# Kernel optimization log

Measured on AMD Instinct MI355X. Metric: run time of the kernel, lower is better.

Reference implementation:

```python
import jax, jax.numpy as jnp
import numpy as np

N_LEVELS = 20
F = 2                      # n_features_per_level
LOG2T = 19
T = 1 << LOG2T             # hashmap size per level
BASE_RES = 16
PER_LEVEL_SCALE = 1.39
N_POINTS = 1_000_000

# 8 corner offsets of a voxel, (8, 3)
OFFSETS = np.array([[i, j, k] for i in (0, 1) for j in (0, 1) for k in (0, 1)], dtype=np.int32)
# spatial hash primes (only 3 needed for 3D input); uint32 multiply wraps like torch int32 bits
PRIME_Y = np.uint32(2654435761)
PRIME_Z = np.uint32(805459861)


def setup_inputs() -> dict:
    key = jax.random.key(0)
    k1, k2 = jax.random.split(key)
    x = jax.random.uniform(k1, (N_POINTS, 3), dtype=jnp.float32)  # points in [0,1)^3
    # nn.init.uniform_(weight, a=-1e-4, b=1e-4), one table per level, stacked
    tables = jax.random.uniform(k2, (N_LEVELS, T, F), minval=-1e-4, maxval=1e-4, dtype=jnp.float32)
    return {"x": x, "tables": tables}


def _hash(coords):
    # coords: (..., 3) int32 voxel corner indices -> (...,) int32 in [0, T)
    c = coords.astype(jnp.uint32)
    h = c[..., 0] ^ (c[..., 1] * PRIME_Y) ^ (c[..., 2] * PRIME_Z)
    return (h & jnp.uint32(T - 1)).astype(jnp.int32)


def _encode_level(x, table, resolution):
    xs = x * resolution                      # (B, 3)
    vmin = jnp.floor(xs).astype(jnp.int32)   # (B, 3)
    corners = vmin[:, None, :] + OFFSETS[None, :, :]   # (B, 8, 3)
    idx = _hash(corners)                     # (B, 8)
    e = table[idx]                           # (B, 8, F) gather
    w = xs - vmin                            # fractional position, (B, 3)
    wx, wy, wz = w[:, 0:1], w[:, 1:2], w[:, 2:3]
    # trilinear interpolation, exact lerp chain from the torch module
    c00 = e[:, 0] * (1 - wx) + e[:, 4] * wx
    c01 = e[:, 1] * (1 - wx) + e[:, 5] * wx
    c10 = e[:, 2] * (1 - wx) + e[:, 6] * wx
    c11 = e[:, 3] * (1 - wx) + e[:, 7] * wx
    c0 = c00 * (1 - wy) + c10 * wy
    c1 = c01 * (1 - wy) + c11 * wy
    return c0 * (1 - wz) + c1 * wz           # (B, F)


def reference(x, tables):
    outs = [_encode_level(x, tables[i], int(BASE_RES * PER_LEVEL_SCALE ** i))
            for i in range(N_LEVELS)]
    return jnp.concatenate(outs, axis=-1)    # (B, N_LEVELS * F) = (B, 40)
```

## Files before the change

### kernel.cpp

```cpp
#include <hip/hip_runtime.h>

#define NLEV 20
#define TSIZE (1u << 19)
#define TMASK (TSIZE - 1u)
#define PRIME_Y 2654435761u
#define PRIME_Z 805459861u

typedef float f32x2 __attribute__((ext_vector_type(2)));
typedef float f32x4 __attribute__((ext_vector_type(4)));

__device__ __constant__ int kRes[NLEV] = {
    16, 22, 30, 42, 59, 83, 115, 160, 222, 309,
    430, 598, 832, 1156, 1608, 2235, 3107, 4318, 6003, 8344};

__device__ __forceinline__ float2 encode_one(const float2* __restrict__ tbl,
                                             float r, float px, float py,
                                             float pz) {
  const float xs0 = px * r, xs1 = py * r, xs2 = pz * r;
  const float f0 = floorf(xs0), f1 = floorf(xs1), f2 = floorf(xs2);
  const float wx = xs0 - f0, wy = xs1 - f1, wz = xs2 - f2;
  const unsigned v0 = (unsigned)(int)f0;
  const unsigned v1 = (unsigned)(int)f1;
  const unsigned v2 = (unsigned)(int)f2;

  const unsigned hy0 = v1 * PRIME_Y, hy1 = (v1 + 1u) * PRIME_Y;
  const unsigned hz0 = v2 * PRIME_Z, hz1 = (v2 + 1u) * PRIME_Z;
  unsigned H[4];
  H[0] = hy0 ^ hz0;
  H[1] = hy0 ^ hz1;
  H[2] = hy1 ^ hz0;
  H[3] = hy1 ^ hz1;

  float2 e0[4], e1[4];

  if ((v0 & 1u) == 0u) {
#pragma unroll
    for (int j = 0; j < 4; ++j) {
      const unsigned i0 = (v0 ^ H[j]) & TMASK;
      const f32x4 q = *(const f32x4*)((const float*)tbl + 2u * (i0 & ~1u));
      const bool lo = (i0 & 1u) == 0u;
      e0[j] = lo ? make_float2(q.x, q.y) : make_float2(q.z, q.w);
      e1[j] = lo ? make_float2(q.z, q.w) : make_float2(q.x, q.y);
    }
  } else {
#pragma unroll
    for (int j = 0; j < 4; ++j) {
      e0[j] = tbl[(v0 ^ H[j]) & TMASK];
      e1[j] = tbl[((v0 + 1u) ^ H[j]) & TMASK];
    }
  }

  const float owx = 1.0f - wx, owy = 1.0f - wy, owz = 1.0f - wz;

  const float c00a = e0[0].x * owx + e1[0].x * wx;
  const float c01a = e0[1].x * owx + e1[1].x * wx;
  const float c10a = e0[2].x * owx + e1[2].x * wx;
  const float c11a = e0[3].x * owx + e1[3].x * wx;
  const float c0a = c00a * owy + c10a * wy;
  const float c1a = c01a * owy + c11a * wy;

  const float c00b = e0[0].y * owx + e1[0].y * wx;
  const float c01b = e0[1].y * owx + e1[1].y * wx;
  const float c10b = e0[2].y * owx + e1[2].y * wx;
  const float c11b = e0[3].y * owx + e1[3].y * wx;
  const float c0b = c00b * owy + c10b * wy;
  const float c1b = c01b * owy + c11b * wy;

  return make_float2(c0a * owz + c1a * wz, c0b * owz + c1b * wz);
}

__global__ __launch_bounds__(256) void enc_level_kernel(
    const float* __restrict__ x, const float* __restrict__ tables,
    float2* __restrict__ ws, int n) {
  const int l = blockIdx.y;
  const int p = blockIdx.x * 256 + threadIdx.x;
  if (p >= n) return;
  const float px = __builtin_nontemporal_load(x + 3 * p + 0);
  const float py = __builtin_nontemporal_load(x + 3 * p + 1);
  const float pz = __builtin_nontemporal_load(x + 3 * p + 2);
  const float2* __restrict__ tbl = (const float2*)tables + (size_t)l * TSIZE;
  const float2 v = encode_one(tbl, (float)kRes[l], px, py, pz);
  f32x2 vv;
  vv.x = v.x;
  vv.y = v.y;
  __builtin_nontemporal_store(vv, (f32x2*)(ws + (size_t)l * n + p));
}

__global__ __launch_bounds__(256) void transpose_kernel(
    const float2* __restrict__ ws, float* __restrict__ out, int n) {
  __shared__ float lds[256 * 41];
  const int p0 = blockIdx.x * 256;
  const int t = threadIdx.x;
  const int npts = min(256, n - p0);

#pragma unroll
  for (int l = 0; l < NLEV; ++l) {
    if (t < npts) {
      const f32x2 v =
          __builtin_nontemporal_load((const f32x2*)(ws + (size_t)l * n + p0 + t));
      lds[t * 41 + 2 * l + 0] = v.x;
      lds[t * 41 + 2 * l + 1] = v.y;
    }
  }
  __syncthreads();

  const int total4 = npts * 10;
  f32x4* __restrict__ dst = (f32x4*)(out + (size_t)p0 * (NLEV * 2));
#pragma unroll
  for (int k = 0; k < 10; ++k) {
    const int g = t + k * 256;
    if (g < total4) {
      const int pl = g / 10;
      const int comp = g - pl * 10;
      const float* s = &lds[pl * 41 + comp * 4];
      f32x4 v;
      v.x = s[0];
      v.y = s[1];
      v.z = s[2];
      v.w = s[3];
      dst[g] = v;
    }
  }
}

__global__ __launch_bounds__(256) void hash_enc_kernel(
    const float* __restrict__ x, const float* __restrict__ tables,
    float* __restrict__ out, int n) {
  int p = blockIdx.x * 256 + threadIdx.x;
  if (p >= n) return;
  const float px = x[3 * p + 0];
  const float py = x[3 * p + 1];
  const float pz = x[3 * p + 2];
  float o[NLEV * 2];
#pragma unroll
  for (int l = 0; l < NLEV; ++l) {
    const float2* tbl = (const float2*)tables + (size_t)l * TSIZE;
    const float2 v = encode_one(tbl, (float)kRes[l], px, py, pz);
    o[2 * l + 0] = v.x;
    o[2 * l + 1] = v.y;
  }
  float4* __restrict__ dst = (float4*)(out + (size_t)p * (NLEV * 2));
#pragma unroll
  for (int k = 0; k < 10; ++k) {
    dst[k] = make_float4(o[4 * k + 0], o[4 * k + 1], o[4 * k + 2], o[4 * k + 3]);
  }
}

extern "C" void kernel_launch(void* const* d_in, const int* in_sizes, int n_in,
                              void* d_out, int out_size, void* d_ws, size_t ws_size,
                              hipStream_t stream) {
  const float* x = (const float*)d_in[0];
  const float* tables = (const float*)d_in[1];
  float* out = (float*)d_out;
  const int n = in_sizes[0] / 3;
  const size_t ws_needed = (size_t)NLEV * n * 2 * sizeof(float);

  if (ws_size >= ws_needed) {
    const int pblocks = (n + 255) / 256;
    dim3 grid1(pblocks, NLEV);
    enc_level_kernel<<<grid1, 256, 0, stream>>>(x, tables, (float2*)d_ws, n);
    transpose_kernel<<<pblocks, 256, 0, stream>>>((const float2*)d_ws, out, n);
  } else {
    const int grid = (n + 255) / 256;
    hash_enc_kernel<<<grid, 256, 0, stream>>>(x, tables, out, n);
  }
}
```

Measured before the change: 685.7 us.

## Unify paired-corner gather path and retile transpose to 128 points per block

```diff
diff --git a/kernel.cpp b/kernel.cpp
--- a/kernel.cpp
+++ b/kernel.cpp
@@ -31,24 +31,26 @@
   H[2] = hy1 ^ hz0;
   H[3] = hy1 ^ hz1;
 
-  float2 e0[4], e1[4];
+  float2 e0[4], epair[4], e1o[4];
 
-  if ((v0 & 1u) == 0u) {
 #pragma unroll
-    for (int j = 0; j < 4; ++j) {
-      const unsigned i0 = (v0 ^ H[j]) & TMASK;
-      const f32x4 q = *(const f32x4*)((const float*)tbl + 2u * (i0 & ~1u));
-      const bool lo = (i0 & 1u) == 0u;
-      e0[j] = lo ? make_float2(q.x, q.y) : make_float2(q.z, q.w);
-      e1[j] = lo ? make_float2(q.z, q.w) : make_float2(q.x, q.y);
-    }
-  } else {
+  for (int j = 0; j < 4; ++j) {
+    const unsigned i0 = (v0 ^ H[j]) & TMASK;
+    const f32x4 q = *(const f32x4*)((const float*)tbl + 2u * (i0 & ~1u));
+    const bool lo = (i0 & 1u) == 0u;
+    e0[j] = lo ? make_float2(q.x, q.y) : make_float2(q.z, q.w);
+    epair[j] = lo ? make_float2(q.z, q.w) : make_float2(q.x, q.y);
+  }
+
+  const bool odd = (v0 & 1u) != 0u;
+  if (odd) {
 #pragma unroll
-    for (int j = 0; j < 4; ++j) {
-      e0[j] = tbl[(v0 ^ H[j]) & TMASK];
-      e1[j] = tbl[((v0 + 1u) ^ H[j]) & TMASK];
-    }
+    for (int j = 0; j < 4; ++j) e1o[j] = tbl[((v0 + 1u) ^ H[j]) & TMASK];
   }
+
+  float2 e1[4];
+#pragma unroll
+  for (int j = 0; j < 4; ++j) e1[j] = odd ? e1o[j] : epair[j];
 
   const float owx = 1.0f - wx, owy = 1.0f - wy, owz = 1.0f - wz;
 
@@ -75,9 +77,9 @@
   const int l = blockIdx.y;
   const int p = blockIdx.x * 256 + threadIdx.x;
   if (p >= n) return;
-  const float px = __builtin_nontemporal_load(x + 3 * p + 0);
-  const float py = __builtin_nontemporal_load(x + 3 * p + 1);
-  const float pz = __builtin_nontemporal_load(x + 3 * p + 2);
+  const float px = x[3 * p + 0];
+  const float py = x[3 * p + 1];
+  const float pz = x[3 * p + 2];
   const float2* __restrict__ tbl = (const float2*)tables + (size_t)l * TSIZE;
   const float2 v = encode_one(tbl, (float)kRes[l], px, py, pz);
   f32x2 vv;
@@ -88,37 +90,39 @@
 
 __global__ __launch_bounds__(256) void transpose_kernel(
     const float2* __restrict__ ws, float* __restrict__ out, int n) {
-  __shared__ float lds[256 * 41];
-  const int p0 = blockIdx.x * 256;
+  __shared__ float lds[128 * 41];
+  const int p0 = blockIdx.x * 128;
   const int t = threadIdx.x;
-  const int npts = min(256, n - p0);
+  const int npts = min(128, n - p0);
 
 #pragma unroll
-  for (int l = 0; l < NLEV; ++l) {
-    if (t < npts) {
+  for (int k = 0; k < 10; ++k) {
+    const int g = t + k * 256;
+    const int l = g >> 7;
+    const int pl = g & 127;
+    if (pl < npts) {
       const f32x2 v =
-          __builtin_nontemporal_load((const f32x2*)(ws + (size_t)l * n + p0 + t));
-      lds[t * 41 + 2 * l + 0] = v.x;
-      lds[t * 41 + 2 * l + 1] = v.y;
+          __builtin_nontemporal_load((const f32x2*)(ws + (size_t)l * n + p0 + pl));
+      lds[pl * 41 + 2 * l + 0] = v.x;
+      lds[pl * 41 + 2 * l + 1] = v.y;
     }
   }
   __syncthreads();
 
-  const int total4 = npts * 10;
   f32x4* __restrict__ dst = (f32x4*)(out + (size_t)p0 * (NLEV * 2));
 #pragma unroll
-  for (int k = 0; k < 10; ++k) {
+  for (int k = 0; k < 5; ++k) {
     const int g = t + k * 256;
-    if (g < total4) {
-      const int pl = g / 10;
-      const int comp = g - pl * 10;
+    const int pl = g / 10;
+    const int comp = g - pl * 10;
+    if (pl < npts) {
       const float* s = &lds[pl * 41 + comp * 4];
       f32x4 v;
       v.x = s[0];
       v.y = s[1];
       v.z = s[2];
       v.w = s[3];
-      dst[g] = v;
+      __builtin_nontemporal_store(v, dst + g);
     }
   }
 }
@@ -159,7 +163,8 @@
     const int pblocks = (n + 255) / 256;
     dim3 grid1(pblocks, NLEV);
     enc_level_kernel<<<grid1, 256, 0, stream>>>(x, tables, (float2*)d_ws, n);
-    transpose_kernel<<<pblocks, 256, 0, stream>>>((const float2*)d_ws, out, n);
+    const int tblocks = (n + 127) / 128;
+    transpose_kernel<<<tblocks, 256, 0, stream>>>((const float2*)d_ws, out, n);
   } else {
     const int grid = (n + 255) / 256;
     hash_enc_kernel<<<grid, 256, 0, stream>>>(x, tables, out, n);
```

Measured after the change: 744.8 us. 1.09x slower.
